# Optimization experiments

Measured on AMD Instinct MI355X. Metric: run time of the kernel, lower is better.

Reference implementation:

```python
import jax, jax.numpy as jnp
import numpy as np

B, N, I = 64, 65536, 8  # batch, nodes, n_blades (2^3 for sig_g=[1,1,1])


def setup_inputs() -> dict:
    key = jax.random.key(0)
    kh, kw = jax.random.split(key)
    h = jax.random.normal(kh, (B, N, I), dtype=jnp.float32)
    W = jax.random.normal(kw, (I, I), dtype=jnp.float32) * 0.1
    return {"h": h, "W": W}


def reference(h, W):
    # E_norm = 0.5 * sum(h^2) over (nodes, blades)
    E_norm = 0.5 * jnp.sum(h * h, axis=(1, 2))
    # h_weighted = h @ W, then interaction term 0.1 * sum(h * hW)
    hW = jnp.einsum('bni,ij->bnj', h, W)
    E_interact = 0.1 * jnp.sum(h * hW, axis=(1, 2))
    return E_norm + E_interact  # shape (B,)
```

## Files before the change

kernel.cpp:

```cpp
#include <hip/hip_runtime.h>


#define B_ 64
#define N_ 65536
#define I_ 8
#define BLOCKS_PER_BATCH 32
#define THREADS 256
#define NODES_PER_BLOCK (N_ / BLOCKS_PER_BATCH)
#define NODES_PER_THREAD (NODES_PER_BLOCK / THREADS)

__global__ __launch_bounds__(THREADS) void energy_partial_kernel(
    const float* __restrict__ h, const float* __restrict__ W,
    float* __restrict__ partial) {
  const int blk = blockIdx.x;
  const int b = blk / BLOCKS_PER_BATCH;
  const int chunk = blk % BLOCKS_PER_BATCH;
  const int t = threadIdx.x;

  float M[I_][I_];
#pragma unroll
  for (int i = 0; i < I_; ++i)
#pragma unroll
    for (int j = 0; j < I_; ++j)
      M[i][j] = 0.1f * W[i * I_ + j] + (i == j ? 0.5f : 0.0f);

  const size_t base = (size_t)b * N_ + (size_t)chunk * NODES_PER_BLOCK;
  float acc = 0.0f;

#pragma unroll
  for (int k = 0; k < NODES_PER_THREAD; ++k) {
    const size_t node = base + (size_t)k * THREADS + (size_t)t;
    const float4* p = reinterpret_cast<const float4*>(h + node * I_);
    float4 a = p[0];
    float4 c = p[1];
    float hv[I_] = {a.x, a.y, a.z, a.w, c.x, c.y, c.z, c.w};
    float e = 0.0f;
#pragma unroll
    for (int i = 0; i < I_; ++i) {
      float ti = 0.0f;
#pragma unroll
      for (int j = 0; j < I_; ++j) ti = fmaf(M[i][j], hv[j], ti);
      e = fmaf(hv[i], ti, e);
    }
    acc += e;
  }

#pragma unroll
  for (int off = 32; off > 0; off >>= 1)
    acc += __shfl_down(acc, off, 64);

  __shared__ float wsum[THREADS / 64];
  const int wave = t >> 6;
  const int lane = t & 63;
  if (lane == 0) wsum[wave] = acc;
  __syncthreads();
  if (t == 0) {
    float s = 0.0f;
#pragma unroll
    for (int w = 0; w < THREADS / 64; ++w) s += wsum[w];
    partial[blk] = s;
  }
}

__global__ void energy_final_kernel(const float* __restrict__ partial,
                                    float* __restrict__ out) {
  const int b = threadIdx.x;
  if (b < B_) {
    float s = 0.0f;
#pragma unroll
    for (int c = 0; c < BLOCKS_PER_BATCH; ++c)
      s += partial[(size_t)b * BLOCKS_PER_BATCH + c];
    out[b] = s;
  }
}

extern "C" void kernel_launch(void* const* d_in, const int* in_sizes, int n_in,
                              void* d_out, int out_size, void* d_ws, size_t ws_size,
                              hipStream_t stream) {
  const float* h = (const float*)d_in[0];
  const float* W = (const float*)d_in[1];
  float* partial = (float*)d_ws;
  float* out = (float*)d_out;

  energy_partial_kernel<<<B_ * BLOCKS_PER_BATCH, THREADS, 0, stream>>>(h, W, partial);
  energy_final_kernel<<<1, 64, 0, stream>>>(partial, out);
}
```

Measured before the change: 26.17 us.

## Symmetrize quadratic form, force uniform coefficients to SGPRs, double blocks per batch

Rewrites the per-node quadratic form h^T M h using the symmetric part of W, so only the diagonal and upper-triangle coefficients are used (36 instead of 64 FMAs per node). Coefficients are passed through readfirstlane so they stay in scalar registers. The grid is doubled to 64 blocks per batch, which halves the nodes per thread and adds parallelism, while the final kernel now sums twice as many partials. The workload is memory-bound (128 MB read), so the arithmetic savings may matter little.

```diff
diff --git a/kernel.cpp b/kernel.cpp
--- a/kernel.cpp
+++ b/kernel.cpp
@@ -4,42 +4,49 @@
 #define B_ 64
 #define N_ 65536
 #define I_ 8
-#define BLOCKS_PER_BATCH 32
+#define BPB 64
 #define THREADS 256
-#define NODES_PER_BLOCK (N_ / BLOCKS_PER_BATCH)
-#define NODES_PER_THREAD (NODES_PER_BLOCK / THREADS)
+#define NPB (N_ / BPB)
+#define NPT (NPB / THREADS)
+
+__device__ __forceinline__ float uniform_f(float x) {
+  return __int_as_float(__builtin_amdgcn_readfirstlane(__float_as_int(x)));
+}
 
 __global__ __launch_bounds__(THREADS) void energy_partial_kernel(
     const float* __restrict__ h, const float* __restrict__ W,
     float* __restrict__ partial) {
   const int blk = blockIdx.x;
-  const int b = blk / BLOCKS_PER_BATCH;
-  const int chunk = blk % BLOCKS_PER_BATCH;
+  const int b = blk >> 6;
+  const int chunk = blk & (BPB - 1);
   const int t = threadIdx.x;
 
-  float M[I_][I_];
+  float c[I_];
+  float s[I_][I_];
 #pragma unroll
-  for (int i = 0; i < I_; ++i)
+  for (int i = 0; i < I_; ++i) {
+    c[i] = uniform_f(0.5f + 0.1f * W[i * I_ + i]);
 #pragma unroll
-    for (int j = 0; j < I_; ++j)
-      M[i][j] = 0.1f * W[i * I_ + j] + (i == j ? 0.5f : 0.0f);
+    for (int j = i + 1; j < I_; ++j)
+      s[i][j] = uniform_f(0.1f * (W[i * I_ + j] + W[j * I_ + i]));
+  }
 
-  const size_t base = (size_t)b * N_ + (size_t)chunk * NODES_PER_BLOCK;
+  const size_t base = (size_t)b * N_ + (size_t)chunk * NPB;
   float acc = 0.0f;
 
 #pragma unroll
-  for (int k = 0; k < NODES_PER_THREAD; ++k) {
+  for (int k = 0; k < NPT; ++k) {
     const size_t node = base + (size_t)k * THREADS + (size_t)t;
     const float4* p = reinterpret_cast<const float4*>(h + node * I_);
     float4 a = p[0];
-    float4 c = p[1];
-    float hv[I_] = {a.x, a.y, a.z, a.w, c.x, c.y, c.z, c.w};
+    float4 d = p[1];
+    float hv[I_] = {a.x, a.y, a.z, a.w, d.x, d.y, d.z, d.w};
     float e = 0.0f;
 #pragma unroll
     for (int i = 0; i < I_; ++i) {
-      float ti = 0.0f;
+      float ti = c[i] * hv[i];
 #pragma unroll
-      for (int j = 0; j < I_; ++j) ti = fmaf(M[i][j], hv[j], ti);
+      for (int j = i + 1; j < I_; ++j) ti = fmaf(s[i][j], hv[j], ti);
       e = fmaf(hv[i], ti, e);
     }
     acc += e;
@@ -55,10 +62,10 @@
   if (lane == 0) wsum[wave] = acc;
   __syncthreads();
   if (t == 0) {
-    float s = 0.0f;
+    float sum = 0.0f;
 #pragma unroll
-    for (int w = 0; w < THREADS / 64; ++w) s += wsum[w];
-    partial[blk] = s;
+    for (int w = 0; w < THREADS / 64; ++w) sum += wsum[w];
+    partial[blk] = sum;
   }
 }
 
@@ -66,11 +73,11 @@
                                     float* __restrict__ out) {
   const int b = threadIdx.x;
   if (b < B_) {
-    float s = 0.0f;
+    float sum = 0.0f;
 #pragma unroll
-    for (int c = 0; c < BLOCKS_PER_BATCH; ++c)
-      s += partial[(size_t)b * BLOCKS_PER_BATCH + c];
-    out[b] = s;
+    for (int c2 = 0; c2 < BPB; ++c2)
+      sum += partial[(size_t)b * BPB + c2];
+    out[b] = sum;
   }
 }
 
@@ -82,6 +89,6 @@
   float* partial = (float*)d_ws;
   float* out = (float*)d_out;
 
-  energy_partial_kernel<<<B_ * BLOCKS_PER_BATCH, THREADS, 0, stream>>>(h, W, partial);
+  energy_partial_kernel<<<B_ * BPB, THREADS, 0, stream>>>(h, W, partial);
   energy_final_kernel<<<1, 64, 0, stream>>>(partial, out);
 }
```

Measured after the change: 26.71 us. 1.02x slower.
